# Kernel tuning notes

Measured on AMD Instinct MI355X. Metric: run time of the kernel, lower is better.

The kernel has to match this reference:

```python
import jax, jax.numpy as jnp
import numpy as np

K = 10          # number of neighbors (init kwarg k)
NUM_CLASSES = 100  # label vocabulary (targets drawn in [0, 100))


def setup_inputs() -> dict:
    key = jax.random.key(0)
    k1, k2, k3 = jax.random.split(key, 3)
    X = jax.random.normal(k1, (1024, 512), dtype=jnp.float32)
    data = jax.random.normal(k2, (50000, 512), dtype=jnp.float32)
    targets = jax.random.randint(k3, (50000,), 0, NUM_CLASSES, dtype=jnp.int64)
    return {"X": X, "data": data, "targets": targets}


def reference(X, data, targets):
    # Pairwise L2 distance (p=2 path of the module), computed via the
    x2 = jnp.sum(X * X, axis=1, keepdims=True)              # [Q, 1]
    d2 = jnp.sum(data * data, axis=1)                        # [N]
    sq = x2 + d2[None, :] - 2.0 * (X @ data.T)               # [Q, N]
    dist = jnp.sqrt(jnp.maximum(sq, 0.0))                    # torch.norm(p1-p2, p=2)

    # torch: sort distances ascending, take first k indices -> top-k smallest.
    _, idx = jax.lax.top_k(-dist, K)                         # [Q, K]
    labels = targets[idx]                                    # [Q, K]

    # torch.mode over the k neighbor labels: histogram + argmax.
    # argmax picks the first (smallest) class on ties, matching torch.mode.
    counts = jax.nn.one_hot(labels, NUM_CLASSES, dtype=jnp.float32).sum(axis=1)  # [Q, C]
    pred = jnp.argmax(counts, axis=1).astype(jnp.float32)    # [Q]
    return pred
```

## Files before the change

kernel.cpp:

```cpp
#include <hip/hip_runtime.h>
#include <math.h>
#include <limits.h>

#define QN 1024
#define NN 50000
#define NPAD 50048
#define DD 512
#define KNN 10
#define NT 128
#define QTB 128
#define BK 32
#define NS 391
#define QB 8
#define NSAMP 31
#define NREST (NS - NSAMP)
#define CAP 512
#define SLACK 4.0f
#define LCAP 1152

#define WS_D2  0
#define WS_TAU 50048
#define WS_CNT (WS_TAU + 1024)
#define WS_XH  (WS_CNT + 1024)
#define WS_CKS (WS_XH + QN * DD / 2)
#define WS_BUF (WS_CKS + QN * NSAMP * KNN * 2)
#define WS_DH  (WS_BUF + QN * CAP * 2)
#define WS_END (WS_DH + NS * 16 * 2048)

typedef __attribute__((ext_vector_type(8))) short short8;
typedef __attribute__((ext_vector_type(4))) float f32x4;
typedef unsigned long long u64;

__device__ __forceinline__ u64 mkkey(float f, int idx) {
  unsigned u = __float_as_uint(f);
  unsigned m = u ^ ((unsigned)((int)u >> 31) | 0x80000000u);
  return ((u64)m << 32) | (unsigned)idx;
}

__device__ __forceinline__ float keyhi_f(unsigned m) {
  unsigned u = (m & 0x80000000u) ? (m ^ 0x80000000u) : ~m;
  return __uint_as_float(u);
}

__device__ __forceinline__ unsigned cvth(float x, float y) {
  unsigned ux = __float_as_uint(x), uy = __float_as_uint(y);
  unsigned rx = ux + 0x7fffu + ((ux >> 16) & 1u);
  unsigned ry = uy + 0x7fffu + ((uy >> 16) & 1u);
  return (rx >> 16) | (ry & 0xffff0000u);
}

__device__ __forceinline__ void ins10(u64* kl, u64 k) {
#pragma unroll
  for (int u = 0; u < KNN; u++) {
    u64 lo = (k < kl[u]) ? k : kl[u];
    u64 hi = (k < kl[u]) ? kl[u] : k;
    kl[u] = lo; k = hi;
  }
}

__global__ __launch_bounds__(256) void conv_kernel(
    const float* __restrict__ dat, const float* __restrict__ Xm,
    float* __restrict__ ws) {
  if ((int)blockIdx.x >= NS) {
    const int g = ((int)blockIdx.x - NS) * 256 + threadIdx.x;
    const int b = g >> 10, kc = (g >> 6) & 15, l = g & 63;
    const int row = b * 16 + (l & 15);
    const int col = kc * 32 + (l >> 4) * 8;
    const float4* p = (const float4*)(Xm + (size_t)row * DD + col);
    float4 v0 = p[0], v1 = p[1];
    ((uint4*)(ws + WS_XH))[g] = make_uint4(
        cvth(v0.x, v0.y), cvth(v0.z, v0.w), cvth(v1.x, v1.y), cvth(v1.z, v1.w));
    return;
  }
  const int slice = blockIdx.x;
  const int t = threadIdx.x;
  const int row = t >> 1, h2 = t & 1;
  const int gr = slice * NT + row;
  const int r15 = row & 15;
  float s = 0.f;
#pragma unroll
  for (int kc8 = 0; kc8 < 8; kc8++) {
    const int kc = h2 * 8 + kc8;
    float4 v[8];
    if (gr < NN) {
      const float4* src = (const float4*)(dat + (size_t)gr * DD + kc * 32);
#pragma unroll
      for (int j = 0; j < 8; j++) v[j] = src[j];
    } else {
#pragma unroll
      for (int j = 0; j < 8; j++) v[j] = make_float4(0.f, 0.f, 0.f, 0.f);
    }
    unsigned hw[16];
#pragma unroll
    for (int j = 0; j < 8; j++) {
      s = fmaf(v[j].x, v[j].x, s); s = fmaf(v[j].y, v[j].y, s);
      s = fmaf(v[j].z, v[j].z, s); s = fmaf(v[j].w, v[j].w, s);
      hw[2 * j]     = cvth(v[j].x, v[j].y);
      hw[2 * j + 1] = cvth(v[j].z, v[j].w);
    }
    uint4* dhp = (uint4*)((unsigned char*)(ws + WS_DH) +
                          (((size_t)slice * 16 + kc) * 8 + (row >> 4)) * 1024);
#pragma unroll
    for (int qd = 0; qd < 4; qd++)
      dhp[qd * 16 + r15] = make_uint4(hw[4 * qd], hw[4 * qd + 1], hw[4 * qd + 2], hw[4 * qd + 3]);
  }
  s += __shfl_xor(s, 1, 64);
  if (h2 == 0) ws[WS_D2 + gr] = (gr < NN) ? s : __builtin_inff();
}

struct StageT { unsigned char bh[8192]; };
struct EpiT  { float sq[64][132]; };
struct ListT { u64 kl[64][4][KNN]; };

template <int PRE, int MODE> struct Smem;
template <> struct Smem<1, 0> { union { EpiT e; ListT l; }; };
template <> struct Smem<1, 1> { float tau[128]; };
template <> struct Smem<0, 0> { union { StageT s; EpiT e; ListT l; }; };
template <> struct Smem<0, 1> { StageT s; float tau[128]; };

template <int PRE, int MODE>
__global__ __launch_bounds__(256, 3) void knn_chunk(
    const float* __restrict__ dat, float* __restrict__ ws, int soff) {
  __shared__ __align__(16) Smem<PRE, MODE> sm;
  int bqx, bsy;
  if (MODE == 1 && (gridDim.y & 7) == 0) {
    const int n = (int)(blockIdx.y * gridDim.x + blockIdx.x);
    const int m = n >> 3;
    const int ypx = (int)(gridDim.y >> 3);
    bqx = m & 7;
    bsy = (n & 7) * ypx + (m >> 3);
  } else {
    bqx = blockIdx.x; bsy = blockIdx.y;
  }
  const int qbase = bqx * QTB;
  const int slice = bsy + soff;
  const int nbase = slice * NT;
  const int t = threadIdx.x;
  const int lane = t & 63, wave = t >> 6;
  const int wn = wave & 1, wq = wave >> 1;
  const unsigned char* dh = (const unsigned char*)(ws + WS_DH);
  const char* xfh = (const char*)(ws + WS_XH);
  const int abase = (((bqx * 8 + wq * 4) * 16) * 64 + lane) * 16;
  const unsigned char* bbase = dh + ((size_t)slice * 16 * 8 + wn * 4) * 1024 + lane * 16;

  f32x4 acc[4][4];
#pragma unroll
  for (int i = 0; i < 4; i++)
#pragma unroll
    for (int j = 0; j < 4; j++) acc[i][j] = (f32x4)0.f;

  if constexpr (PRE == 1) {
    short8 ca[4], cb[4];
#pragma unroll
    for (int i = 0; i < 4; i++) {
      ca[i] = *(const short8*)(xfh + abase + i * 16384);
      cb[i] = *(const short8*)(bbase + i * 1024);
    }
#pragma unroll
    for (int kc = 0; kc < 16; kc++) {
      short8 na[4], nb[4];
      if (kc < 15) {
#pragma unroll
        for (int i = 0; i < 4; i++) {
          na[i] = *(const short8*)(xfh + abase + i * 16384 + (kc + 1) * 1024);
          nb[i] = *(const short8*)(bbase + ((kc + 1) * 8 + i) * 1024);
        }
      }
#pragma unroll
      for (int mt = 0; mt < 4; mt++)
#pragma unroll
        for (int nt = 0; nt < 4; nt++)
          acc[mt][nt] = __builtin_amdgcn_mfma_f32_16x16x32_bf16(ca[mt], cb[nt], acc[mt][nt], 0, 0, 0);
      if (kc < 15) {
#pragma unroll
        for (int i = 0; i < 4; i++) { ca[i] = na[i]; cb[i] = nb[i]; }
      }
    }
  } else {
    const int brow = t >> 1, bh_half = t & 1;
    const int bgr = nbase + brow;
    const int bpanel = (brow >> 4) * 1024;
    const int bchunk = (brow & 15) * 16;
    for (int kc = 0; kc < 16; kc++) {
      const int kk = kc * BK;
      short8 fah[4];
#pragma unroll
      for (int i = 0; i < 4; i++)
        fah[i] = *(const short8*)(xfh + abase + i * 16384 + kc * 1024);
      __syncthreads();
      {
        float4 v0 = make_float4(0.f, 0.f, 0.f, 0.f), v1 = v0, v2 = v0, v3 = v0;
        if (bgr < NN) {
          const float4* src = (const float4*)(dat + (size_t)bgr * DD + kk + bh_half * 16);
          v0 = src[0]; v1 = src[1]; v2 = src[2]; v3 = src[3];
        }
        unsigned char* bhp = sm.s.bh + bpanel;
        *(uint4*)(bhp + (2 * bh_half) * 256 + bchunk) =
            make_uint4(cvth(v0.x, v0.y), cvth(v0.z, v0.w), cvth(v1.x, v1.y), cvth(v1.z, v1.w));
        *(uint4*)(bhp + (2 * bh_half + 1) * 256 + bchunk) =
            make_uint4(cvth(v2.x, v2.y), cvth(v2.z, v2.w), cvth(v3.x, v3.y), cvth(v3.z, v3.w));
      }
      __syncthreads();
      const int fragoff = lane * 16;
      short8 fbh[4];
#pragma unroll
      for (int i = 0; i < 4; i++)
        fbh[i] = *(const short8*)(sm.s.bh + (wn * 4 + i) * 1024 + fragoff);
      __syncthreads();
#pragma unroll
      for (int mt = 0; mt < 4; mt++)
#pragma unroll
        for (int nt = 0; nt < 4; nt++)
          acc[mt][nt] = __builtin_amdgcn_mfma_f32_16x16x32_bf16(fah[mt], fbh[nt], acc[mt][nt], 0, 0, 0);
    }
  }

  if constexpr (MODE == 0) {
#pragma unroll
    for (int pass = 0; pass < 2; pass++) {
      __syncthreads();
      if (wq == pass) {
#pragma unroll
        for (int nt = 0; nt < 4; nt++) {
          int col = wn * 64 + nt * 16 + (lane & 15);
          float d2v = ws[WS_D2 + nbase + col];
#pragma unroll
          for (int mt = 0; mt < 4; mt++)
#pragma unroll
            for (int rg = 0; rg < 4; rg++) {
              int lr = mt * 16 + (lane >> 4) * 4 + rg;
              sm.e.sq[lr][col] = fmaf(-2.f, acc[mt][nt][rg], d2v);
            }
        }
      }
      __syncthreads();
      {
        const int r = t >> 2, s = t & 3;
        u64 kl[KNN];
#pragma unroll
        for (int u = 0; u < KNN; u++) kl[u] = ~0ull;
        for (int jj = 0; jj < 32; jj++) {
          int c = s * 32 + ((jj + r + 8 * s) & 31);
          float v = sm.e.sq[r][c];
          ins10(kl, mkkey(v, nbase + c));
        }
        __syncthreads();
#pragma unroll
        for (int u = 0; u < KNN; u++) sm.l.kl[r][s][u] = kl[u];
      }
      __syncthreads();
      if (t < 64) {
        u64* dst = ((u64*)(ws + WS_CKS)) +
                   ((size_t)(qbase + pass * 64 + t) * NSAMP + blockIdx.y) * KNN;
        int h0 = 0, h1 = 0, h2 = 0, h3 = 0;
        for (int pick = 0; pick < KNN; pick++) {
          u64 k0 = sm.l.kl[t][0][h0], k1 = sm.l.kl[t][1][h1];
          u64 k2 = sm.l.kl[t][2][h2], k3 = sm.l.kl[t][3][h3];
          u64 best = k0; int bm = 0;
          if (k1 < best) { best = k1; bm = 1; }
          if (k2 < best) { best = k2; bm = 2; }
          if (k3 < best) { best = k3; bm = 3; }
          dst[pick] = best;
          h0 += (bm == 0); h1 += (bm == 1); h2 += (bm == 2); h3 += (bm == 3);
        }
      }
    }
  } else {
    if (t < 128) sm.tau[t] = ws[WS_TAU + qbase + t];
    __syncthreads();
    unsigned* cnt = (unsigned*)(ws + WS_CNT);
    u64* buf = (u64*)(ws + WS_BUF);
    float d2v[4];
#pragma unroll
    for (int nt = 0; nt < 4; nt++)
      d2v[nt] = ws[WS_D2 + nbase + wn * 64 + nt * 16 + (lane & 15)];
#pragma unroll
    for (int mt = 0; mt < 4; mt++)
#pragma unroll
      for (int rg = 0; rg < 4; rg++) {
        int row = wq * 64 + mt * 16 + (lane >> 4) * 4 + rg;
        float tr = sm.tau[row];
#pragma unroll
        for (int nt = 0; nt < 4; nt++) {
          float d = fmaf(-2.f, acc[mt][nt][rg], d2v[nt]);
          if (d < tr) {
            int col = nbase + wn * 64 + nt * 16 + (lane & 15);
            int q = qbase + row;
            unsigned slot = atomicAdd(cnt + q, 1u);
            if (slot < CAP) buf[(size_t)q * CAP + slot] = mkkey(d, col);
          }
        }
      }
  }
}

__global__ __launch_bounds__(64) void tau_kernel(float* __restrict__ ws) {
  const int q = blockIdx.x;
  const int t = threadIdx.x;
  const u64* samp = ((const u64*)(ws + WS_CKS)) + (size_t)q * NSAMP * KNN;
  const int NC = NSAMP * KNN;
  u64 kl[KNN];
#pragma unroll
  for (int u = 0; u < KNN; u++) kl[u] = ~0ull;
  for (int j = t; j < NC; j += 64) ins10(kl, samp[j]);
  __shared__ u64 wk[64][KNN];
  __shared__ u64 m2[8][KNN];
#pragma unroll
  for (int u = 0; u < KNN; u++) wk[t][u] = kl[u];
  __syncthreads();
  if (t < 8) {
    int h[8] = {0, 0, 0, 0, 0, 0, 0, 0};
    for (int pick = 0; pick < KNN; pick++) {
      u64 best = ~0ull; int bm = 0;
#pragma unroll
      for (int m = 0; m < 8; m++) {
        u64 km = wk[t * 8 + m][h[m]];
        if (km < best) { best = km; bm = m; }
      }
      m2[t][pick] = best;
#pragma unroll
      for (int m = 0; m < 8; m++) h[m] += (bm == m);
    }
  }
  __syncthreads();
  if (t == 0) {
    int h[8] = {0, 0, 0, 0, 0, 0, 0, 0};
    u64 best = 0;
    for (int pick = 0; pick < KNN; pick++) {
      best = ~0ull; int bm = 0;
#pragma unroll
      for (int m = 0; m < 8; m++) {
        u64 km = m2[m][h[m]];
        if (km < best) { best = km; bm = m; }
      }
#pragma unroll
      for (int m = 0; m < 8; m++) h[m] += (bm == m);
    }
    ws[WS_TAU + q] = keyhi_f((unsigned)(best >> 32)) + SLACK;
    ((unsigned*)(ws + WS_CNT))[q] = 0u;
  }
}

__global__ __launch_bounds__(256) void knn_final(
    const int* __restrict__ targets, const float* __restrict__ Xm,
    const float* __restrict__ dat, float* __restrict__ ws,
    float* __restrict__ out) {
  const int q = blockIdx.x;
  const int t = threadIdx.x;
  const int lane = t & 63, wave = t >> 6;
  __shared__ float qrow[DD];
  __shared__ unsigned lst[LCAP];
  __shared__ int nlist;
  __shared__ u64 wk4[4][KNN];
  if (t == 0) nlist = 0;
  if (t < 128) ((float4*)qrow)[t] = ((const float4*)(Xm + (size_t)q * DD))[t];
  __syncthreads();
  const float tr = ws[WS_TAU + q];
  const u64* samp = ((const u64*)(ws + WS_CKS)) + (size_t)q * NSAMP * KNN;
  for (int j = t; j < NSAMP * KNN; j += 256) {
    u64 k = samp[j];
    if (keyhi_f((unsigned)(k >> 32)) < tr) {
      int s_ = atomicAdd(&nlist, 1);
      if (s_ < LCAP) lst[s_] = (unsigned)k;
    }
  }
  unsigned c = ((const unsigned*)(ws + WS_CNT))[q];
  if (c > CAP) c = CAP;
  const u64* buf = ((const u64*)(ws + WS_BUF)) + (size_t)q * CAP;
  for (int j = t; j < (int)c; j += 256) {
    int s_ = atomicAdd(&nlist, 1);
    if (s_ < LCAP) lst[s_] = (unsigned)buf[j];
  }
  __syncthreads();
  const int n = nlist < LCAP ? nlist : LCAP;

  u64 kl[KNN];
#pragma unroll
  for (int u = 0; u < KNN; u++) kl[u] = ~0ull;
  const float4* qv = (const float4*)qrow;
  const float4 q0 = qv[lane * 2], q1 = qv[lane * 2 + 1];
  for (int j = wave; j < n; j += 8) {
    const unsigned i0 = lst[j];
    const int has1 = (j + 4) < n;
    const unsigned i1 = has1 ? lst[j + 4] : i0;
    const float4* x0 = (const float4*)(dat + (size_t)i0 * DD) + lane * 2;
    const float4* x1 = (const float4*)(dat + (size_t)i1 * DD) + lane * 2;
    const float4 a0 = x0[0], a1 = x0[1];
    const float4 b0 = x1[0], b1 = x1[1];
    float p0 = a0.x * q0.x, p1 = b0.x * q0.x;
    p0 = fmaf(a0.y, q0.y, p0); p1 = fmaf(b0.y, q0.y, p1);
    p0 = fmaf(a0.z, q0.z, p0); p1 = fmaf(b0.z, q0.z, p1);
    p0 = fmaf(a0.w, q0.w, p0); p1 = fmaf(b0.w, q0.w, p1);
    p0 = fmaf(a1.x, q1.x, p0); p1 = fmaf(b1.x, q1.x, p1);
    p0 = fmaf(a1.y, q1.y, p0); p1 = fmaf(b1.y, q1.y, p1);
    p0 = fmaf(a1.z, q1.z, p0); p1 = fmaf(b1.z, q1.z, p1);
    p0 = fmaf(a1.w, q1.w, p0); p1 = fmaf(b1.w, q1.w, p1);
#pragma unroll
    for (int s_ = 1; s_ < 64; s_ <<= 1) {
      p0 += __shfl_xor(p0, s_, 64);
      p1 += __shfl_xor(p1, s_, 64);
    }
    float d0 = fmaf(-2.f, p0, ws[WS_D2 + i0]);
    u64 k0 = mkkey(d0, (int)i0);
    if (k0 < kl[KNN - 1]) ins10(kl, k0);
    if (has1) {
      float d1 = fmaf(-2.f, p1, ws[WS_D2 + i1]);
      u64 k1 = mkkey(d1, (int)i1);
      if (k1 < kl[KNN - 1]) ins10(kl, k1);
    }
  }
  if (lane == 0)
#pragma unroll
    for (int u = 0; u < KNN; u++) wk4[wave][u] = kl[u];
  __syncthreads();
  if (t == 0) {
    int h[4] = {0, 0, 0, 0};
    int fi[KNN];
    for (int pick = 0; pick < KNN; pick++) {
      u64 best = ~0ull; int bm = 0;
#pragma unroll
      for (int m = 0; m < 4; m++) {
        u64 km = wk4[m][h[m]];
        if (km < best) { best = km; bm = m; }
      }
      fi[pick] = (int)(unsigned)(best & 0xffffffffu);
      h[bm]++;
    }
    int lab[KNN];
#pragma unroll
    for (int u = 0; u < KNN; u++) lab[u] = targets[fi[u]];
    int bc = 0, bl = INT_MAX;
#pragma unroll
    for (int i = 0; i < KNN; i++) {
      int cc = 0;
#pragma unroll
      for (int j = 0; j < KNN; j++) cc += (lab[j] == lab[i]) ? 1 : 0;
      if (cc > bc || (cc == bc && lab[i] < bl)) { bc = cc; bl = lab[i]; }
    }
    out[q] = (float)bl;
  }
}

extern "C" void kernel_launch(void* const* d_in, const int* in_sizes, int n_in,
                              void* d_out, int out_size, void* d_ws, size_t ws_size,
                              hipStream_t stream) {
  const float* Xm  = (const float*)d_in[0];
  const float* dat = (const float*)d_in[1];
  const int* targets = (const int*)d_in[2];
  float* out = (float*)d_out;
  float* ws  = (float*)d_ws;
  const bool pre = ws_size >= (size_t)WS_END * 4;

  hipLaunchKernelGGL(conv_kernel, dim3(NS + QN * DD / 8 / 256), dim3(256), 0,
                     stream, dat, Xm, ws);
  if (pre) {
    hipLaunchKernelGGL((knn_chunk<1, 0>), dim3(QB, NSAMP), dim3(256), 0, stream, dat, ws, 0);
    hipLaunchKernelGGL(tau_kernel, dim3(QN), dim3(64), 0, stream, ws);
    hipLaunchKernelGGL((knn_chunk<1, 1>), dim3(QB, NREST), dim3(256), 0, stream, dat, ws, NSAMP);
  } else {
    hipLaunchKernelGGL((knn_chunk<0, 0>), dim3(QB, NSAMP), dim3(256), 0, stream, dat, ws, 0);
    hipLaunchKernelGGL(tau_kernel, dim3(QN), dim3(64), 0, stream, ws);
    hipLaunchKernelGGL((knn_chunk<0, 1>), dim3(QB, NREST), dim3(256), 0, stream, dat, ws, NSAMP);
  }
  hipLaunchKernelGGL(knn_final, dim3(QN), dim3(256), 0, stream, targets, Xm, dat, ws, out);
}
```

Measured before the change: 367.5 us.

## Stage pre-converted bf16 tiles through LDS with global_load_lds in PRE path

In the pre-converted path, A and B bf16 fragments are no longer loaded straight from global memory into registers with register double-buffering. Each wave now issues direct global-to-LDS loads (global_load_lds) for its share of the A and B panels. All waves then read their MFMA fragments from shared memory, so each panel is fetched from global memory once per block instead of once per wave that uses it. The cost is two barriers per k-step and a larger staging buffer in shared memory, which may reduce occupancy in MODE 1.

```diff
diff --git a/kernel.cpp b/kernel.cpp
--- a/kernel.cpp
+++ b/kernel.cpp
@@ -49,6 +49,12 @@
   return (rx >> 16) | (ry & 0xffff0000u);
 }
 
+__device__ __forceinline__ void glds16(const void* g, void* l) {
+  __builtin_amdgcn_global_load_lds(
+      (const __attribute__((address_space(1))) unsigned*)g,
+      (__attribute__((address_space(3))) unsigned*)l, 16, 0, 0);
+}
+
 __device__ __forceinline__ void ins10(u64* kl, u64 k) {
 #pragma unroll
   for (int u = 0; u < KNN; u++) {
@@ -108,20 +114,21 @@
   if (h2 == 0) ws[WS_D2 + gr] = (gr < NN) ? s : __builtin_inff();
 }
 
-struct StageT { unsigned char bh[8192]; };
+struct StageT { unsigned char ah[8192], bh[8192]; };
 struct EpiT  { float sq[64][132]; };
 struct ListT { u64 kl[64][4][KNN]; };
 
-template <int PRE, int MODE> struct Smem;
-template <> struct Smem<1, 0> { union { EpiT e; ListT l; }; };
-template <> struct Smem<1, 1> { float tau[128]; };
-template <> struct Smem<0, 0> { union { StageT s; EpiT e; ListT l; }; };
-template <> struct Smem<0, 1> { StageT s; float tau[128]; };
+template <int MODE> struct SmemSel {
+  union U { StageT s; EpiT e; ListT l; };
+};
+template <> struct SmemSel<1> {
+  struct U { StageT s; float tau[128]; };
+};
 
 template <int PRE, int MODE>
 __global__ __launch_bounds__(256, 3) void knn_chunk(
     const float* __restrict__ dat, float* __restrict__ ws, int soff) {
-  __shared__ __align__(16) Smem<PRE, MODE> sm;
+  __shared__ __align__(16) typename SmemSel<MODE>::U sm;
   int bqx, bsy;
   if (MODE == 1 && (gridDim.y & 7) == 0) {
     const int n = (int)(blockIdx.y * gridDim.x + blockIdx.x);
@@ -140,8 +147,6 @@
   const int wn = wave & 1, wq = wave >> 1;
   const unsigned char* dh = (const unsigned char*)(ws + WS_DH);
   const char* xfh = (const char*)(ws + WS_XH);
-  const int abase = (((bqx * 8 + wq * 4) * 16) * 64 + lane) * 16;
-  const unsigned char* bbase = dh + ((size_t)slice * 16 * 8 + wn * 4) * 1024 + lane * 16;
 
   f32x4 acc[4][4];
 #pragma unroll
@@ -149,34 +154,44 @@
 #pragma unroll
     for (int j = 0; j < 4; j++) acc[i][j] = (f32x4)0.f;
 
-  if constexpr (PRE == 1) {
-    short8 ca[4], cb[4];
-#pragma unroll
-    for (int i = 0; i < 4; i++) {
-      ca[i] = *(const short8*)(xfh + abase + i * 16384);
-      cb[i] = *(const short8*)(bbase + i * 1024);
-    }
-#pragma unroll
+  auto stage = [&](int kc) {
+#pragma unroll
+    for (int i = 0; i < 2; i++) {
+      int pp = wave * 2 + i;
+      const char* ga = xfh +
+          ((((size_t)(bqx * 8 + pp) * 16 + kc) * 64) + lane) * 16;
+      glds16(ga, sm.s.ah + pp * 1024);
+    }
+#pragma unroll
+    for (int i = 0; i < 2; i++) {
+      int p = wave * 2 + i;
+      const unsigned char* gb = dh +
+          (((size_t)slice * 16 + kc) * 8 + p) * 1024 + lane * 16;
+      glds16(gb, sm.s.bh + p * 1024);
+    }
+  };
+
+  if (PRE) {
+    stage(0);
     for (int kc = 0; kc < 16; kc++) {
-      short8 na[4], nb[4];
-      if (kc < 15) {
-#pragma unroll
-        for (int i = 0; i < 4; i++) {
-          na[i] = *(const short8*)(xfh + abase + i * 16384 + (kc + 1) * 1024);
-          nb[i] = *(const short8*)(bbase + ((kc + 1) * 8 + i) * 1024);
-        }
-      }
+      __syncthreads();
+      const int fragoff = lane * 16;
+      short8 fah[4], fbh[4];
+#pragma unroll
+      for (int i = 0; i < 4; i++) {
+        fah[i] = *(const short8*)(sm.s.ah + (wq * 4 + i) * 1024 + fragoff);
+        fbh[i] = *(const short8*)(sm.s.bh + (wn * 4 + i) * 1024 + fragoff);
+      }
+      __syncthreads();
+      if (kc < 15) stage(kc + 1);
 #pragma unroll
       for (int mt = 0; mt < 4; mt++)
 #pragma unroll
         for (int nt = 0; nt < 4; nt++)
-          acc[mt][nt] = __builtin_amdgcn_mfma_f32_16x16x32_bf16(ca[mt], cb[nt], acc[mt][nt], 0, 0, 0);
-      if (kc < 15) {
-#pragma unroll
-        for (int i = 0; i < 4; i++) { ca[i] = na[i]; cb[i] = nb[i]; }
-      }
+          acc[mt][nt] = __builtin_amdgcn_mfma_f32_16x16x32_bf16(fah[mt], fbh[nt], acc[mt][nt], 0, 0, 0);
     }
   } else {
+    const int abase = (((bqx * 8 + wq * 4) * 16) * 64 + lane) * 16;
     const int brow = t >> 1, bh_half = t & 1;
     const int bgr = nbase + brow;
     const int bpanel = (brow >> 4) * 1024;
```

Measured after the change: 335.2 us. 1.1x faster.
